# Optimization experiments

Measured on AMD Instinct MI355X. Metric: run time of the kernel, lower is better.

Reference implementation:

```python
import jax, jax.numpy as jnp
import numpy as np

T = 2048
HIDDEN = 4096
NQ = 32
NKV = 8
HD = 128
THETA = 10000.0


def setup_inputs() -> dict:
    key = jax.random.key(0)
    ks = jax.random.split(key, 5)
    s = 1.0 / np.sqrt(HIDDEN)
    return {
        "positions": jnp.arange(T, dtype=jnp.int32),
        "hidden_states": jax.random.normal(ks[0], (T, HIDDEN), dtype=jnp.float32),
        "wq": jax.random.normal(ks[1], (HIDDEN, NQ * HD), dtype=jnp.float32) * s,
        "wk": jax.random.normal(ks[2], (HIDDEN, NKV * HD), dtype=jnp.float32) * s,
        "wv": jax.random.normal(ks[3], (HIDDEN, NKV * HD), dtype=jnp.float32) * s,
        "wo": jax.random.normal(ks[4], (NQ * HD, HIDDEN), dtype=jnp.float32) * s,
    }


def _rope_neox(x, positions):
    # x: [T, H, HD]; neox style: split halves, rotate
    half = HD // 2
    inv_freq = 1.0 / (THETA ** (jnp.arange(0, half, dtype=jnp.float32) / half))
    ang = positions.astype(jnp.float32)[:, None] * inv_freq[None, :]  # [T, half]
    cos = jnp.cos(ang)[:, None, :]  # [T, 1, half]
    sin = jnp.sin(ang)[:, None, :]
    x1, x2 = x[..., :half], x[..., half:]
    return jnp.concatenate([x1 * cos - x2 * sin, x2 * cos + x1 * sin], axis=-1)


def reference(positions, hidden_states, wq, wk, wv, wo):
    scale = HD ** -0.5
    q = (hidden_states @ wq).reshape(T, NQ, HD)
    k = (hidden_states @ wk).reshape(T, NKV, HD)
    v = (hidden_states @ wv).reshape(T, NKV, HD)
    q = _rope_neox(q, positions)
    k = _rope_neox(k, positions)
    # GQA: repeat kv heads to match q heads
    group = NQ // NKV
    k_r = jnp.repeat(k, group, axis=1)  # [T, NQ, HD]
    v_r = jnp.repeat(v, group, axis=1)
    scores = jnp.einsum('qhd,khd->hqk', q, k_r) * scale  # [NQ, T, T]
    causal = positions[:, None] >= positions[None, :]  # [T, T]
    scores = jnp.where(causal[None, :, :], scores, -jnp.inf)
    probs = jax.nn.softmax(scores, axis=-1)
    attn = jnp.einsum('hqk,khd->qhd', probs, v_r).reshape(T, NQ * HD)
    return attn @ wo
```

## Files before the change

### kernel.cpp

```cpp
#include <hip/hip_runtime.h>

#define T_SEQ  2048
#define HID    4096
#define NQH    32
#define NKVH   8
#define HDIM   128

typedef float  f32x4  __attribute__((ext_vector_type(4)));
typedef __bf16 bf16x8 __attribute__((ext_vector_type(8)));

__device__ __forceinline__ float bf2f(unsigned short u) {
  union { unsigned int i; float f; } v; v.i = ((unsigned int)u) << 16; return v.f;
}
__device__ __forceinline__ unsigned short f2bf(float f) {
  union { float f; unsigned int i; } v; v.f = f;
  unsigned int r = v.i + 0x7fffu + ((v.i >> 16) & 1u);
  return (unsigned short)(r >> 16);
}

__device__ __forceinline__ f32x4 mfma_bf16(bf16x8 a, bf16x8 b, f32x4 c) {
  return __builtin_amdgcn_mfma_f32_16x16x32_bf16(a, b, c, 0, 0, 0);
}

#define GLOAD16(g, l)                                              \
  __builtin_amdgcn_global_load_lds(                                \
      (const __attribute__((address_space(1))) void*)(g),          \
      (__attribute__((address_space(3))) void*)(l), 16, 0, 0)

__global__ void conv_f32_bf16(const float* __restrict__ in,
                              unsigned short* __restrict__ out) {
  long long i = ((long long)blockIdx.x * 256 + threadIdx.x) * 4;
  float4 v = *(const float4*)(in + i);
  union { unsigned short u[4]; uint2 p; } o;
  o.u[0] = f2bf(v.x); o.u[1] = f2bf(v.y); o.u[2] = f2bf(v.z); o.u[3] = f2bf(v.w);
  *(uint2*)(out + i) = o.p;
}

__global__ void transpose_conv(const float* __restrict__ W,
                               unsigned short* __restrict__ Wt, int K, int N) {
  __shared__ float tile[64][65];
  int n0 = blockIdx.x * 64, k0 = blockIdx.y * 64;
  int tx = threadIdx.x & 15, ty = threadIdx.x >> 4;
#pragma unroll
  for (int i = 0; i < 4; i++) {
    int k = ty + 16 * i;
    float4 f = *(const float4*)(W + (long long)(k0 + k) * N + n0 + tx * 4);
    tile[tx * 4 + 0][k] = f.x;
    tile[tx * 4 + 1][k] = f.y;
    tile[tx * 4 + 2][k] = f.z;
    tile[tx * 4 + 3][k] = f.w;
  }
  __syncthreads();
#pragma unroll
  for (int i = 0; i < 4; i++) {
    int n = ty + 16 * i;
    union { unsigned short u[4]; uint2 p; } o;
    o.u[0] = f2bf(tile[n][tx * 4 + 0]);
    o.u[1] = f2bf(tile[n][tx * 4 + 1]);
    o.u[2] = f2bf(tile[n][tx * 4 + 2]);
    o.u[3] = f2bf(tile[n][tx * 4 + 3]);
    *(uint2*)(Wt + (long long)(n0 + n) * K + k0 + tx * 4) = o.p;
  }
}

__global__ void transpose_conv_kv(const float* __restrict__ Wk,
                                  const float* __restrict__ Wv,
                                  unsigned short* __restrict__ Wt) {
  __shared__ float tile[64][65];
  const int N = NKVH * HDIM, K = HID;
  const float* W = blockIdx.z ? Wv : Wk;
  unsigned short* dst = Wt + (size_t)blockIdx.z * N * K;
  int n0 = blockIdx.x * 64, k0 = blockIdx.y * 64;
  int tx = threadIdx.x & 15, ty = threadIdx.x >> 4;
#pragma unroll
  for (int i = 0; i < 4; i++) {
    int k = ty + 16 * i;
    float4 f = *(const float4*)(W + (long long)(k0 + k) * N + n0 + tx * 4);
    tile[tx * 4 + 0][k] = f.x;
    tile[tx * 4 + 1][k] = f.y;
    tile[tx * 4 + 2][k] = f.z;
    tile[tx * 4 + 3][k] = f.w;
  }
  __syncthreads();
#pragma unroll
  for (int i = 0; i < 4; i++) {
    int n = ty + 16 * i;
    union { unsigned short u[4]; uint2 p; } o;
    o.u[0] = f2bf(tile[n][tx * 4 + 0]);
    o.u[1] = f2bf(tile[n][tx * 4 + 1]);
    o.u[2] = f2bf(tile[n][tx * 4 + 2]);
    o.u[3] = f2bf(tile[n][tx * 4 + 3]);
    *(uint2*)(dst + (long long)(n0 + n) * K + k0 + tx * 4) = o.p;
  }
}

template <int EPI>
__global__ __launch_bounds__(256) void gemm_bt(const unsigned short* __restrict__ A,
                                               const unsigned short* __restrict__ Bt,
                                               void* __restrict__ Cv,
                                               int M, int N, int K) {
  __shared__ unsigned short As[128 * 64];
  __shared__ unsigned short Bs[128 * 64];
  const int lin = blockIdx.y * gridDim.x + blockIdx.x;
  const int cpx = (gridDim.x * gridDim.y) >> 3;
  const int swz = (lin & 7) * cpx + (lin >> 3);
  const int bx = swz % gridDim.x, by = swz / gridDim.x;

  const int t = threadIdx.x;
  const int lane = t & 63, w = t >> 6;
  const int wr = w >> 1, wc = w & 1;
  const int l15 = lane & 15, lg = lane >> 4;
  const int m0 = by * 128, n0 = bx * 128;

  f32x4 acc[4][4];
#pragma unroll
  for (int i = 0; i < 4; i++)
#pragma unroll
    for (int j = 0; j < 4; j++) acc[i][j] = (f32x4){0.f, 0.f, 0.f, 0.f};

  for (int kt = 0; kt < K; kt += 64) {
    __syncthreads();
#pragma unroll
    for (int s = 0; s < 4; s++) {
      int c = t + s * 256;
      int row = c >> 3, sub = c & 7;
      GLOAD16(A + (long long)(m0 + row) * K + kt + ((sub ^ (row & 7)) * 8),
              (char*)As + (w * 64 + s * 256) * 16);
      GLOAD16(Bt + (long long)(n0 + row) * K + kt + ((sub ^ (row & 7)) * 8),
              (char*)Bs + (w * 64 + s * 256) * 16);
    }
    __syncthreads();

#pragma unroll
    for (int kk = 0; kk < 2; kk++) {
      bf16x8 af[4], bfr[4];
#pragma unroll
      for (int mi = 0; mi < 4; mi++) {
        int row = wr * 64 + mi * 16 + l15;
        af[mi] = *(const bf16x8*)(As + row * 64 + (((kk * 4 + lg) ^ (row & 7)) * 8));
      }
#pragma unroll
      for (int ni = 0; ni < 4; ni++) {
        int row = wc * 64 + ni * 16 + l15;
        bfr[ni] = *(const bf16x8*)(Bs + row * 64 + (((kk * 4 + lg) ^ (row & 7)) * 8));
      }
#pragma unroll
      for (int mi = 0; mi < 4; mi++)
#pragma unroll
        for (int ni = 0; ni < 4; ni++)
          acc[mi][ni] = mfma_bf16(af[mi], bfr[ni], acc[mi][ni]);
    }
  }

  const int row0 = m0 + wr * 64, col0 = n0 + wc * 64;
#pragma unroll
  for (int mi = 0; mi < 4; mi++)
#pragma unroll
    for (int ni = 0; ni < 4; ni++) {
      int rbase = row0 + mi * 16 + lg * 4;
      int col = col0 + ni * 16 + l15;
#pragma unroll
      for (int r = 0; r < 4; r++) {
        float v = acc[mi][ni][r];
        if (EPI == 0)
          ((unsigned short*)Cv)[(long long)(rbase + r) * N + col] = f2bf(v);
        else
          ((float*)Cv)[(long long)(rbase + r) * N + col] = v;
      }
    }
}

__global__ __launch_bounds__(256) void gemm_kv64(const unsigned short* __restrict__ A,
                                                 const unsigned short* __restrict__ Bt,
                                                 unsigned short* __restrict__ Ckv,
                                                 unsigned short* __restrict__ Cvt) {
  __shared__ unsigned short As[64 * 64];
  __shared__ unsigned short Bs[128 * 64];
  __shared__ unsigned short Tt[128 * 64];
  const int lin = blockIdx.y * gridDim.x + blockIdx.x;
  const int swz = (lin & 7) * 64 + (lin >> 3);
  const int bx = swz & 15, by = swz >> 4;

  const int t = threadIdx.x;
  const int lane = t & 63, w = t >> 6;
  const int wr = w >> 1, wc = w & 1;
  const int l15 = lane & 15, lg = lane >> 4;
  const int m0 = by * 64, n0 = bx * 128;
  const int K = HID;

  f32x4 acc[2][4];
#pragma unroll
  for (int i = 0; i < 2; i++)
#pragma unroll
    for (int j = 0; j < 4; j++) acc[i][j] = (f32x4){0.f, 0.f, 0.f, 0.f};

  for (int kt = 0; kt < K; kt += 64) {
    __syncthreads();
#pragma unroll
    for (int s = 0; s < 2; s++) {
      int c = t + s * 256;
      int row = c >> 3, sub = c & 7;
      GLOAD16(A + (long long)(m0 + row) * K + kt + ((sub ^ (row & 7)) * 8),
              (char*)As + (w * 64 + s * 256) * 16);
    }
#pragma unroll
    for (int s = 0; s < 4; s++) {
      int c = t + s * 256;
      int row = c >> 3, sub = c & 7;
      GLOAD16(Bt + (long long)(n0 + row) * K + kt + ((sub ^ (row & 7)) * 8),
              (char*)Bs + (w * 64 + s * 256) * 16);
    }
    __syncthreads();

#pragma unroll
    for (int kk = 0; kk < 2; kk++) {
      bf16x8 af[2], bfr[4];
#pragma unroll
      for (int mi = 0; mi < 2; mi++) {
        int row = wr * 32 + mi * 16 + l15;
        af[mi] = *(const bf16x8*)(As + row * 64 + (((kk * 4 + lg) ^ (row & 7)) * 8));
      }
#pragma unroll
      for (int ni = 0; ni < 4; ni++) {
        int row = wc * 64 + ni * 16 + l15;
        bfr[ni] = *(const bf16x8*)(Bs + row * 64 + (((kk * 4 + lg) ^ (row & 7)) * 8));
      }
#pragma unroll
      for (int mi = 0; mi < 2; mi++)
#pragma unroll
        for (int ni = 0; ni < 4; ni++)
          acc[mi][ni] = mfma_bf16(af[mi], bfr[ni], acc[mi][ni]);
    }
  }

  const int row0 = m0 + wr * 32, col0 = n0 + wc * 64;
  if (n0 < 1024) {
#pragma unroll
    for (int mi = 0; mi < 2; mi++)
#pragma unroll
      for (int ni = 0; ni < 4; ni++) {
        int rbase = row0 + mi * 16 + lg * 4;
        int col = col0 + ni * 16 + l15;
#pragma unroll
        for (int r = 0; r < 4; r++)
          Ckv[(long long)(rbase + r) * 1024 + col] = f2bf(acc[mi][ni][r]);
      }
  } else {
#pragma unroll
    for (int mi = 0; mi < 2; mi++)
#pragma unroll
      for (int ni = 0; ni < 4; ni++) {
        int nloc = wc * 64 + ni * 16 + l15;
#pragma unroll
        for (int r = 0; r < 4; r++) {
          int mloc = wr * 32 + mi * 16 + lg * 4 + r;
          Tt[nloc * 64 + (mloc ^ ((nloc & 7) << 3))] = f2bf(acc[mi][ni][r]);
        }
      }
    __syncthreads();
    const int nloc = t >> 1;
#pragma unroll
    for (int cc = 0; cc < 4; cc++) {
      int ci = (t & 1) * 4 + cc;
      int sc = ci ^ (nloc & 7);
      uint4 v = *(const uint4*)(Tt + nloc * 64 + sc * 8);
      *(uint4*)(Cvt + (long long)(n0 - 1024 + nloc) * T_SEQ + m0 + ci * 8) = v;
    }
  }
}

__global__ void rope_all(unsigned short* __restrict__ qb,
                         unsigned short* __restrict__ kb,
                         const int* __restrict__ positions) {
  const int w = threadIdx.x >> 6, d = threadIdx.x & 63;
  const int gid = blockIdx.x * 4 + w;
  unsigned short* row;
  int t;
  bool isq;
  if (gid < T_SEQ * NQH) {
    int h = gid & (NQH - 1); t = gid >> 5;
    row = qb + (size_t)t * (NQH * HDIM) + (size_t)h * HDIM;
    isq = true;
  } else {
    int g = gid - T_SEQ * NQH;
    int h = g & (NKVH - 1); t = g >> 3;
    row = kb + (size_t)t * (NKVH * HDIM) + (size_t)h * HDIM;
    isq = false;
  }
  double inv = exp2(-(double)d * 0.20762050593046014);
  double ang = (double)positions[t] * inv;
  double c = cos(ang), s = sin(ang);
  if (isq) { c *= 0.12751744416986895; s *= 0.12751744416986895; }
  float x1 = bf2f(row[d]), x2 = bf2f(row[d + 64]);
  row[d]      = f2bf((float)((double)x1 * c - (double)x2 * s));
  row[d + 64] = f2bf((float)((double)x2 * c + (double)x1 * s));
}

__global__ __launch_bounds__(256) void attn_kernel(const unsigned short* __restrict__ qb,
                                                   const unsigned short* __restrict__ kb,
                                                   const unsigned short* __restrict__ vt,
                                                   unsigned short* __restrict__ ab) {
  __shared__ unsigned short Ks[64 * 128];
  __shared__ unsigned short Vs[128 * 64];
  __shared__ unsigned short Ps[4][16 * 64];

  const int lin = blockIdx.y * gridDim.x + blockIdx.x;
  const int swz = (lin & 7) * 128 + (lin >> 3);
  const int bx = swz & 31;
  const int h  = swz >> 5;
  const int kvh = h >> 2;
  const int j  = (h & 1) ? bx : 31 - bx;
  const int q0 = j * 64;
  const int t = threadIdx.x, lane = t & 63, w = t >> 6;
  const int l15 = lane & 15, lg = lane >> 4;

  bf16x8 qf[4];
#pragma unroll
  for (int kk = 0; kk < 4; kk++)
    qf[kk] = *(const bf16x8*)(qb + (long long)(q0 + w * 16 + l15) * (NQH * HDIM) +
                              h * HDIM + kk * 32 + lg * 8);

  f32x4 accO[8];
#pragma unroll
  for (int db = 0; db < 8; db++) accO[db] = (f32x4){0.f, 0.f, 0.f, 0.f};
  float mrun[4] = {-3e38f, -3e38f, -3e38f, -3e38f};
  float lrun[4] = {0.f, 0.f, 0.f, 0.f};

  const int nt = j + 1;
  for (int kt = 0; kt < nt; kt++) {
    __syncthreads();
#pragma unroll
    for (int s = 0; s < 4; s++) {
      int c = t + s * 256;
      int row = c >> 4, chk = c & 15;
      GLOAD16(kb + (long long)(kt * 64 + row) * (NKVH * HDIM) + kvh * HDIM +
                  ((chk ^ (row & 7)) * 8),
              (char*)Ks + (w * 64 + s * 256) * 16);
    }
#pragma unroll
    for (int s = 0; s < 4; s++) {
      int c = t + s * 256;
      int row = c >> 3, chk = c & 7;
      GLOAD16(vt + (long long)(kvh * HDIM + row) * T_SEQ + kt * 64 +
                  ((chk ^ (row & 7)) * 8),
              (char*)Vs + (w * 64 + s * 256) * 16);
    }
    __syncthreads();

    f32x4 accS[4];
#pragma unroll
    for (int kc = 0; kc < 4; kc++) accS[kc] = (f32x4){0.f, 0.f, 0.f, 0.f};
    __builtin_amdgcn_s_setprio(1);
#pragma unroll
    for (int kk = 0; kk < 4; kk++)
#pragma unroll
      for (int kc = 0; kc < 4; kc++) {
        int row = kc * 16 + l15;
        bf16x8 b = *(const bf16x8*)(Ks + row * 128 + (((kk * 4 + lg) ^ (l15 & 7)) * 8));
        accS[kc] = mfma_bf16(qf[kk], b, accS[kc]);
      }
    __builtin_amdgcn_s_setprio(0);

    float pm[4][4];
    if (kt == j) {
#pragma unroll
      for (int kc = 0; kc < 4; kc++) {
        int kcl = kc * 16 + l15;
#pragma unroll
        for (int r = 0; r < 4; r++)
          pm[kc][r] = (kcl > w * 16 + lg * 4 + r) ? -3e38f : accS[kc][r];
      }
    } else {
#pragma unroll
      for (int kc = 0; kc < 4; kc++)
#pragma unroll
        for (int r = 0; r < 4; r++) pm[kc][r] = accS[kc][r];
    }

    float rm[4];
#pragma unroll
    for (int r = 0; r < 4; r++)
      rm[r] = fmaxf(fmaxf(pm[0][r], pm[1][r]), fmaxf(pm[2][r], pm[3][r]));
    int needl = 0;
#pragma unroll
    for (int r = 0; r < 4; r++) needl |= (rm[r] > mrun[r] + 8.f) ? 1 : 0;
    if (__any(needl)) {
#pragma unroll
      for (int off = 1; off < 16; off <<= 1)
#pragma unroll
        for (int r = 0; r < 4; r++) rm[r] = fmaxf(rm[r], __shfl_xor(rm[r], off, 64));
#pragma unroll
      for (int r = 0; r < 4; r++) {
        float mn = fmaxf(mrun[r], rm[r]);
        float corr = exp2f(mrun[r] - mn);
        mrun[r] = mn;
        lrun[r] *= corr;
#pragma unroll
        for (int db = 0; db < 8; db++) accO[db][r] *= corr;
      }
    }

    __bf16 pbh[4][4];
#pragma unroll
    for (int kc = 0; kc < 4; kc++)
#pragma unroll
      for (int r = 0; r < 4; r++) {
        float p = exp2f(pm[kc][r] - mrun[r]);
        lrun[r] += p;
        pbh[kc][r] = (__bf16)p;
      }

    unsigned short* Pw = &Ps[w][0];
#pragma unroll
    for (int kc = 0; kc < 4; kc++)
#pragma unroll
      for (int r = 0; r < 4; r++) {
        int prow = lg * 4 + r;
        ((__bf16*)Pw)[(prow * 64 + kc * 16 + l15) ^ ((prow & 7) << 3)] = pbh[kc][r];
      }
    asm volatile("s_waitcnt lgkmcnt(0)" ::: "memory");

    __builtin_amdgcn_s_setprio(1);
#pragma unroll
    for (int ks = 0; ks < 2; ks++) {
      bf16x8 pa = *(const bf16x8*)(Pw + ((l15 * 64 + ks * 32 + lg * 8) ^ ((l15 & 7) << 3)));
#pragma unroll
      for (int db = 0; db < 8; db++) {
        int vrow = db * 16 + l15;
        bf16x8 b = *(const bf16x8*)(Vs + vrow * 64 + (((ks * 4 + lg) ^ (l15 & 7)) * 8));
        accO[db] = mfma_bf16(pa, b, accO[db]);
      }
    }
    __builtin_amdgcn_s_setprio(0);
  }

#pragma unroll
  for (int off = 1; off < 16; off <<= 1)
#pragma unroll
    for (int r = 0; r < 4; r++) lrun[r] += __shfl_xor(lrun[r], off, 64);
#pragma unroll
  for (int db = 0; db < 8; db++)
#pragma unroll
    for (int r = 0; r < 4; r++) {
      int qr = q0 + w * 16 + lg * 4 + r;
      int col = h * HDIM + db * 16 + l15;
      ((__bf16*)ab)[(long long)qr * (NQH * HDIM) + col] = (__bf16)(accO[db][r] / lrun[r]);
    }
}

extern "C" void kernel_launch(void* const* d_in, const int* in_sizes, int n_in,
                              void* d_out, int out_size, void* d_ws, size_t ws_size,
                              hipStream_t stream) {
  const int*   positions = (const int*)d_in[0];
  const float* hs = (const float*)d_in[1];
  const float* wq = (const float*)d_in[2];
  const float* wk = (const float*)d_in[3];
  const float* wv = (const float*)d_in[4];
  const float* wo = (const float*)d_in[5];
  float* out = (float*)d_out;

  const size_t SZ_WT = (size_t)HID * HID * 2;
  const size_t SZ_HB = (size_t)T_SEQ * HID * 2;
  const size_t SZ_QB = (size_t)T_SEQ * NQH * HDIM * 2;
  const size_t SZ_KB = (size_t)T_SEQ * NKVH * HDIM * 2;
  const size_t need = SZ_WT + SZ_HB + SZ_QB + SZ_KB * 2;
  if (ws_size < need) return;

  char* p = (char*)d_ws;
  unsigned short* wt  = (unsigned short*)p; p += SZ_WT;
  unsigned short* hb  = (unsigned short*)p; p += SZ_HB;
  unsigned short* qb  = (unsigned short*)p; p += SZ_QB;
  unsigned short* kb  = (unsigned short*)p; p += SZ_KB;
  unsigned short* vtb = (unsigned short*)p; p += SZ_KB;
  unsigned short* ab  = hb;

  conv_f32_bf16<<<(T_SEQ * HID) / 1024, 256, 0, stream>>>(hs, hb);

  transpose_conv<<<dim3((NQH * HDIM) / 64, HID / 64), 256, 0, stream>>>(wq, wt, HID, NQH * HDIM);
  gemm_bt<0><<<dim3((NQH * HDIM) / 128, T_SEQ / 128), 256, 0, stream>>>(hb, wt, qb, T_SEQ, NQH * HDIM, HID);

  transpose_conv_kv<<<dim3((NKVH * HDIM) / 64, HID / 64, 2), 256, 0, stream>>>(wk, wv, wt);
  gemm_kv64<<<dim3(16, 32), 256, 0, stream>>>(hb, wt, kb, vtb);

  rope_all<<<(T_SEQ * (NQH + NKVH)) / 4, 256, 0, stream>>>(qb, kb, positions);

  attn_kernel<<<dim3(32, 32), 256, 0, stream>>>(qb, kb, vtb, ab);

  transpose_conv<<<dim3(HID / 64, (NQH * HDIM) / 64), 256, 0, stream>>>(wo, wt, NQH * HDIM, HID);
  gemm_bt<2><<<dim3(HID / 128, T_SEQ / 128), 256, 0, stream>>>(ab, wt, out, T_SEQ, HID, NQH * HDIM);
}
```

Measured before the change: 399.9 us.

## Load K/V fragments directly from global in attention; fuse hidden and Wq prep kernels

```diff
diff --git a/kernel.cpp b/kernel.cpp
--- a/kernel.cpp
+++ b/kernel.cpp
@@ -27,13 +27,41 @@
       (const __attribute__((address_space(1))) void*)(g),          \
       (__attribute__((address_space(3))) void*)(l), 16, 0, 0)
 
-__global__ void conv_f32_bf16(const float* __restrict__ in,
-                              unsigned short* __restrict__ out) {
-  long long i = ((long long)blockIdx.x * 256 + threadIdx.x) * 4;
-  float4 v = *(const float4*)(in + i);
-  union { unsigned short u[4]; uint2 p; } o;
-  o.u[0] = f2bf(v.x); o.u[1] = f2bf(v.y); o.u[2] = f2bf(v.z); o.u[3] = f2bf(v.w);
-  *(uint2*)(out + i) = o.p;
+__global__ void prep_qw(const float* __restrict__ hs, unsigned short* __restrict__ hb,
+                        const float* __restrict__ wq, unsigned short* __restrict__ wt) {
+  __shared__ float tile[64][65];
+  if (blockIdx.x < 8192) {
+    long long i = ((long long)blockIdx.x * 256 + threadIdx.x) * 4;
+    float4 v = *(const float4*)(hs + i);
+    union { unsigned short u[4]; uint2 p; } o;
+    o.u[0] = f2bf(v.x); o.u[1] = f2bf(v.y); o.u[2] = f2bf(v.z); o.u[3] = f2bf(v.w);
+    *(uint2*)(hb + i) = o.p;
+    return;
+  }
+  const int bid = blockIdx.x - 8192;
+  const int N = NQH * HDIM, K = HID;
+  int n0 = (bid & 63) * 64, k0 = (bid >> 6) * 64;
+  int tx = threadIdx.x & 15, ty = threadIdx.x >> 4;
+#pragma unroll
+  for (int i = 0; i < 4; i++) {
+    int k = ty + 16 * i;
+    float4 f = *(const float4*)(wq + (long long)(k0 + k) * N + n0 + tx * 4);
+    tile[tx * 4 + 0][k] = f.x;
+    tile[tx * 4 + 1][k] = f.y;
+    tile[tx * 4 + 2][k] = f.z;
+    tile[tx * 4 + 3][k] = f.w;
+  }
+  __syncthreads();
+#pragma unroll
+  for (int i = 0; i < 4; i++) {
+    int n = ty + 16 * i;
+    union { unsigned short u[4]; uint2 p; } o;
+    o.u[0] = f2bf(tile[n][tx * 4 + 0]);
+    o.u[1] = f2bf(tile[n][tx * 4 + 1]);
+    o.u[2] = f2bf(tile[n][tx * 4 + 2]);
+    o.u[3] = f2bf(tile[n][tx * 4 + 3]);
+    *(uint2*)(wt + (long long)(n0 + n) * K + k0 + tx * 4) = o.p;
+  }
 }
 
 __global__ void transpose_conv(const float* __restrict__ W,
@@ -300,8 +328,6 @@
                                                    const unsigned short* __restrict__ kb,
                                                    const unsigned short* __restrict__ vt,
                                                    unsigned short* __restrict__ ab) {
-  __shared__ unsigned short Ks[64 * 128];
-  __shared__ unsigned short Vs[128 * 64];
   __shared__ unsigned short Ps[4][16 * 64];
 
   const int lin = blockIdx.y * gridDim.x + blockIdx.x;
@@ -314,6 +340,9 @@
   const int t = threadIdx.x, lane = t & 63, w = t >> 6;
   const int l15 = lane & 15, lg = lane >> 4;
 
+  const unsigned short* kbase = kb + (size_t)l15 * (NKVH * HDIM) + kvh * HDIM + lg * 8;
+  const unsigned short* vbase = vt + (size_t)(kvh * HDIM + l15) * T_SEQ + lg * 8;
+
   bf16x8 qf[4];
 #pragma unroll
   for (int kk = 0; kk < 4; kk++)
@@ -328,37 +357,21 @@
 
   const int nt = j + 1;
   for (int kt = 0; kt < nt; kt++) {
-    __syncthreads();
-#pragma unroll
-    for (int s = 0; s < 4; s++) {
-      int c = t + s * 256;
-      int row = c >> 4, chk = c & 15;
-      GLOAD16(kb + (long long)(kt * 64 + row) * (NKVH * HDIM) + kvh * HDIM +
-                  ((chk ^ (row & 7)) * 8),
-              (char*)Ks + (w * 64 + s * 256) * 16);
-    }
-#pragma unroll
-    for (int s = 0; s < 4; s++) {
-      int c = t + s * 256;
-      int row = c >> 3, chk = c & 7;
-      GLOAD16(vt + (long long)(kvh * HDIM + row) * T_SEQ + kt * 64 +
-                  ((chk ^ (row & 7)) * 8),
-              (char*)Vs + (w * 64 + s * 256) * 16);
-    }
-    __syncthreads();
-
     f32x4 accS[4];
 #pragma unroll
     for (int kc = 0; kc < 4; kc++) accS[kc] = (f32x4){0.f, 0.f, 0.f, 0.f};
     __builtin_amdgcn_s_setprio(1);
 #pragma unroll
-    for (int kk = 0; kk < 4; kk++)
-#pragma unroll
-      for (int kc = 0; kc < 4; kc++) {
-        int row = kc * 16 + l15;
-        bf16x8 b = *(const bf16x8*)(Ks + row * 128 + (((kk * 4 + lg) ^ (l15 & 7)) * 8));
-        accS[kc] = mfma_bf16(qf[kk], b, accS[kc]);
-      }
+    for (int kc = 0; kc < 4; kc++) {
+      const unsigned short* kr = kbase + (size_t)(kt * 64 + kc * 16) * (NKVH * HDIM);
+      bf16x8 kf[4];
+#pragma unroll
+      for (int kk = 0; kk < 4; kk++)
+        kf[kk] = *(const bf16x8*)(kr + kk * 32);
+#pragma unroll
+      for (int kk = 0; kk < 4; kk++)
+        accS[kc] = mfma_bf16(qf[kk], kf[kk], accS[kc]);
+    }
     __builtin_amdgcn_s_setprio(0);
 
     float pm[4][4];
@@ -426,8 +439,7 @@
       bf16x8 pa = *(const bf16x8*)(Pw + ((l15 * 64 + ks * 32 + lg * 8) ^ ((l15 & 7) << 3)));
 #pragma unroll
       for (int db = 0; db < 8; db++) {
-        int vrow = db * 16 + l15;
-        bf16x8 b = *(const bf16x8*)(Vs + vrow * 64 + (((ks * 4 + lg) ^ (l15 & 7)) * 8));
+        bf16x8 b = *(const bf16x8*)(vbase + (size_t)db * 16 * T_SEQ + kt * 64 + ks * 32);
         accO[db] = mfma_bf16(pa, b, accO[db]);
       }
     }
@@ -474,9 +486,7 @@
   unsigned short* vtb = (unsigned short*)p; p += SZ_KB;
   unsigned short* ab  = hb;
 
-  conv_f32_bf16<<<(T_SEQ * HID) / 1024, 256, 0, stream>>>(hs, hb);
-
-  transpose_conv<<<dim3((NQH * HDIM) / 64, HID / 64), 256, 0, stream>>>(wq, wt, HID, NQH * HDIM);
+  prep_qw<<<8192 + 4096, 256, 0, stream>>>(hs, hb, wq, wt);
   gemm_bt<0><<<dim3((NQH * HDIM) / 128, T_SEQ / 128), 256, 0, stream>>>(hb, wt, qb, T_SEQ, NQH * HDIM, HID);
 
   transpose_conv_kv<<<dim3((NKVH * HDIM) / 64, HID / 64, 2), 256, 0, stream>>>(wk, wv, wt);
```

Result: slower. 624.7 us (+56.2%).
